# Kernel optimization log

Hardware: AMD Instinct MI355X
Metric: run time of the kernel (lower is better)

## Reference

```python
import jax, jax.numpy as jnp
import numpy as np

B, C, H, W = 8, 256, 128, 128
NUM_HEADS = 8
EPS = 1e-6


def setup_inputs() -> dict:
    key = jax.random.key(0)
    ks = jax.random.split(key, 7)
    s = 1.0 / np.sqrt(C)
    return {
        "x": jax.random.normal(ks[0], (B, C, H, W), dtype=jnp.float32),
        "Wq": jax.random.normal(ks[1], (C, C), dtype=jnp.float32) * s,
        "bq": jax.random.normal(ks[2], (C,), dtype=jnp.float32) * 0.01,
        "Wk": jax.random.normal(ks[3], (C, C), dtype=jnp.float32) * s,
        "bk": jax.random.normal(ks[4], (C,), dtype=jnp.float32) * 0.01,
        "Wv": jax.random.normal(ks[5], (C, C), dtype=jnp.float32) * s,
        "bv": jax.random.normal(ks[6], (C,), dtype=jnp.float32) * 0.01,
    }


def reference(x, Wq, bq, Wk, bk, Wv, bv):
    b, c_full, h_sp, w_sp = x.shape
    p = NUM_HEADS
    c = c_full // p  # per-head channels
    n = h_sp * w_sp  # spatial tokens

    def proj(Wm, bm):
        # 1x1 conv == channel-mixing linear: out[b,o,h,w] = sum_c W[o,c]*x[b,c,h,w] + b[o]
        return jnp.einsum('bchw,oc->bohw', x, Wm) + bm[None, :, None, None]

    q = jax.nn.softplus(proj(Wq, bq)).reshape(b, p, c, n).transpose(0, 1, 3, 2)  # [b,p,n,c]
    k = jax.nn.softplus(proj(Wk, bk)).reshape(b, p, c, n)                        # [b,p,c,n]
    v = proj(Wv, bv).reshape(b, p, c, n)                                         # [b,p,c,n]

    # KV accumulation: [b,p,c_k,c_v] (small)
    kv = jnp.einsum('bpmn,bpcn->bpmc', k, v)
    # normalization: 1 / (q . (sum_n k + eps))
    norm = 1.0 / jnp.einsum('bpnc,bpc->bpn', q, jnp.sum(k, axis=-1) + EPS)
    out = jnp.einsum('bpnm,bpmc,bpn->bpcn', q, kv, norm)  # [b,p,c,n]
    return out.reshape(b, c_full, h_sp, w_sp)
```

## Files before the change

kernel.cpp:

```cpp
#include <hip/hip_runtime.h>
#include <hip/hip_bf16.h>
#include <math.h>

#define BATCH 8
#define CFULL 256
#define HEADS 8
#define CH 32
#define NTOK 16384
#define TN 64
#define EPS 1e-6f

#define SWZ(tok) ((((tok) & 7) << 3) ^ ((((tok) >> 3) & 3) << 6))

typedef __bf16 bf16x8 __attribute__((ext_vector_type(8)));
typedef float f32x4 __attribute__((ext_vector_type(4)));
typedef float f32x16 __attribute__((ext_vector_type(16)));
typedef float fvec4 __attribute__((ext_vector_type(4)));
typedef unsigned short ushort8v __attribute__((ext_vector_type(8)));
typedef int int4v __attribute__((ext_vector_type(4)));

__device__ __forceinline__ unsigned short bf16bits(float f) {
    return __builtin_bit_cast(unsigned short, (__bf16)f);
}
__device__ __forceinline__ float softplus_f(float x) {
    return fmaxf(x, 0.0f) + __logf(1.0f + __expf(-fabsf(x)));
}

__device__ __forceinline__ void quad_transpose(fvec4& a, int lane) {
    const bool o1 = lane & 1, o2 = lane & 2;
    float s1 = o1 ? a.x : a.y; float g1 = __shfl_xor(s1, 1);
    float s2 = o1 ? a.z : a.w; float g2 = __shfl_xor(s2, 1);
    a.x = o1 ? g1 : a.x;  a.y = o1 ? a.y : g1;
    a.z = o1 ? g2 : a.z;  a.w = o1 ? a.w : g2;
    float s3 = o2 ? a.x : a.z; float g3 = __shfl_xor(s3, 2);
    float s4 = o2 ? a.y : a.w; float g4 = __shfl_xor(s4, 2);
    a.x = o2 ? g3 : a.x;  a.z = o2 ? a.z : g3;
    a.y = o2 ? g4 : a.y;  a.w = o2 ? a.w : g4;
}

template <int NW>
__device__ __forceinline__ void stage_x(const float* __restrict__ xb, int n0,
                                        unsigned short* xs, int wv, int lane) {
    const int q4 = lane & 3;
    const int t0 = (lane >> 2) << 2;
    constexpr int G = 64 / NW;
    #pragma unroll
    for (int g = 0; g < G; ++g) {
        const int c0 = wv * (G * 4) + g * 4;
        fvec4 a = __builtin_nontemporal_load(
            (const fvec4*)(xb + (size_t)(c0 + q4) * NTOK + n0 + t0));
        quad_transpose(a, lane);
        ushort4 pk;
        pk.x = bf16bits(a.x); pk.y = bf16bits(a.y);
        pk.z = bf16bits(a.z); pk.w = bf16bits(a.w);
        *(ushort4*)&xs[lane * CFULL + (c0 ^ SWZ(lane))] = pk;
    }
}

template <int NW>
__device__ __forceinline__ void stage_tile(const unsigned short* __restrict__ xTb,
                                           int n0, unsigned short* xs, int wv, int lane) {
    constexpr int R = 64 / NW;
    const unsigned short* src = xTb + (size_t)(n0 + wv * R) * CFULL + lane * 8;
    unsigned short* dst = &xs[wv * R * CFULL];
    #pragma unroll
    for (int i = 0; i < R / 2; ++i) {
        __builtin_amdgcn_global_load_lds(
            (const __attribute__((address_space(1))) unsigned int*)(src + i * 512),
            (__attribute__((address_space(3))) unsigned int*)(dst + i * 512),
            16, 0, 0);
    }
}

__global__ void prep_w(const float* __restrict__ Wq, const float* __restrict__ Wk,
                       const float* __restrict__ Wv, unsigned short* __restrict__ dst)
{
    const int i = blockIdx.x * 256 + threadIdx.x;
    const float* src = (i < 65536) ? Wq : ((i < 131072) ? Wk : Wv);
    dst[i] = bf16bits(src[i & 65535]);
}

__global__ __launch_bounds__(512)
void xpose(const float* __restrict__ x, unsigned short* __restrict__ xT)
{
    __shared__ __align__(16) unsigned short xs[TN * CFULL];
    const int tid = threadIdx.x;
    const int lane = tid & 63;
    const int wv = tid >> 6;
    const int b = blockIdx.x >> 8;
    const int n0 = (blockIdx.x & 255) * TN;

    stage_x<8>(x + (size_t)b * CFULL * NTOK, n0, xs, wv, lane);
    __syncthreads();
    int4v* dst = (int4v*)(xT + ((size_t)b * NTOK + n0) * CFULL);
    const int4v* src = (const int4v*)xs;
    #pragma unroll
    for (int i = 0; i < 4; ++i)
        dst[i * 512 + tid] = src[i * 512 + tid];
}

__global__ __launch_bounds__(512)
void k1_kv(const unsigned short* __restrict__ xT,
           const unsigned short* __restrict__ Wk,
           const unsigned short* __restrict__ Wv,
           const float* __restrict__ bk, const float* __restrict__ bv,
           float* __restrict__ kvpart, float* __restrict__ kspart,
           int bpb, int ntiles)
{
    __shared__ __align__(16) unsigned short xs[TN * CFULL];
    __shared__ __align__(16) unsigned short ks[CFULL * TN];

    const int tid = threadIdx.x;
    const int lane = tid & 63;
    const int wv = tid >> 6;
    const int l15 = lane & 15;
    const int lhi = lane >> 4;
    const int bid = blockIdx.x;
    const int b = bid / bpb;
    const int blk = bid % bpb;
    const unsigned short* xTb = xT + (size_t)b * NTOK * CFULL;

    float bkr[2], bvr[2];
    #pragma unroll
    for (int of = 0; of < 2; ++of) {
        bkr[of] = bk[wv * 32 + of * 16 + l15];
        bvr[of] = bv[wv * 32 + of * 16 + l15];
    }

    f32x16 kvacc = {};
    float ksum[2] = {0.f, 0.f};

    for (int t = 0; t < ntiles; ++t) {
        const int n0 = (blk * ntiles + t) * TN;
        __syncthreads();
        stage_tile<8>(xTb, n0, xs, wv, lane);
        __syncthreads();

        #pragma unroll
        for (int tfh = 0; tfh < 2; ++tfh) {
            f32x4 acc[2][2] = {};
            #pragma unroll
            for (int kk = 0; kk < 8; ++kk) {
                const int ch0 = kk * 32 + lhi * 8;
                bf16x8 af[2], bfr[2];
                #pragma unroll
                for (int tf = 0; tf < 2; ++tf) {
                    const int tok = (tfh * 2 + tf) * 16 + l15;
                    af[tf] = *(const bf16x8*)&xs[tok * CFULL + (ch0 ^ SWZ(tok))];
                }
                #pragma unroll
                for (int of = 0; of < 2; ++of) {
                    const int och = wv * 32 + of * 16 + l15;
                    bfr[of] = *(const bf16x8*)&Wk[och * CFULL + ch0];
                }
                #pragma unroll
                for (int tf = 0; tf < 2; ++tf)
                    #pragma unroll
                    for (int of = 0; of < 2; ++of)
                        acc[tf][of] = __builtin_amdgcn_mfma_f32_16x16x32_bf16(af[tf], bfr[of], acc[tf][of], 0, 0, 0);
            }
            #pragma unroll
            for (int tf = 0; tf < 2; ++tf) {
                #pragma unroll
                for (int of = 0; of < 2; ++of) {
                    const int och = wv * 32 + of * 16 + l15;
                    const float bias = bkr[of];
                    float v0 = softplus_f(acc[tf][of][0] + bias);
                    float v1 = softplus_f(acc[tf][of][1] + bias);
                    float v2 = softplus_f(acc[tf][of][2] + bias);
                    float v3 = softplus_f(acc[tf][of][3] + bias);
                    ksum[of] += v0 + v1 + v2 + v3;
                    ushort4 pk;
                    pk.x = bf16bits(v0); pk.y = bf16bits(v1);
                    pk.z = bf16bits(v2); pk.w = bf16bits(v3);
                    const int tok0 = (tfh * 2 + tf) * 16 + lhi * 4;
                    *(ushort4*)&ks[och * TN + (tok0 ^ ((och & 7) << 3))] = pk;
                }
            }
        }

        ushort4 vpk[4][2];
        #pragma unroll
        for (int tfh = 0; tfh < 2; ++tfh) {
            f32x4 acc[2][2] = {};
            #pragma unroll
            for (int kk = 0; kk < 8; ++kk) {
                const int ch0 = kk * 32 + lhi * 8;
                bf16x8 af[2], bfr[2];
                #pragma unroll
                for (int tf = 0; tf < 2; ++tf) {
                    const int tok = (tfh * 2 + tf) * 16 + l15;
                    af[tf] = *(const bf16x8*)&xs[tok * CFULL + (ch0 ^ SWZ(tok))];
                }
                #pragma unroll
                for (int of = 0; of < 2; ++of) {
                    const int och = wv * 32 + of * 16 + l15;
                    bfr[of] = *(const bf16x8*)&Wv[och * CFULL + ch0];
                }
                #pragma unroll
                for (int tf = 0; tf < 2; ++tf)
                    #pragma unroll
                    for (int of = 0; of < 2; ++of)
                        acc[tf][of] = __builtin_amdgcn_mfma_f32_16x16x32_bf16(af[tf], bfr[of], acc[tf][of], 0, 0, 0);
            }
            #pragma unroll
            for (int tf = 0; tf < 2; ++tf)
                #pragma unroll
                for (int of = 0; of < 2; ++of) {
                    const float bias = bvr[of];
                    vpk[tfh * 2 + tf][of].x = bf16bits(acc[tf][of][0] + bias);
                    vpk[tfh * 2 + tf][of].y = bf16bits(acc[tf][of][1] + bias);
                    vpk[tfh * 2 + tf][of].z = bf16bits(acc[tf][of][2] + bias);
                    vpk[tfh * 2 + tf][of].w = bf16bits(acc[tf][of][3] + bias);
                }
        }
        __syncthreads();
        #pragma unroll
        for (int tf = 0; tf < 4; ++tf)
            #pragma unroll
            for (int of = 0; of < 2; ++of) {
                const int och = wv * 32 + of * 16 + l15;
                const int tok0 = tf * 16 + lhi * 4;
                *(ushort4*)&xs[och * TN + (tok0 ^ ((och & 7) << 3))] = vpk[tf][of];
            }

        {
            const int l31 = lane & 31;
            const int tb = (lane >> 5) * 8;
            const int row = wv * 32 + l31;
            #pragma unroll
            for (int ts = 0; ts < 4; ++ts) {
                const int sw = (ts * 16 + tb) ^ ((row & 7) << 3);
                bf16x8 ak = *(const bf16x8*)&ks[row * TN + sw];
                bf16x8 av = *(const bf16x8*)&xs[row * TN + sw];
                kvacc = __builtin_amdgcn_mfma_f32_32x32x16_bf16(ak, av, kvacc, 0, 0, 0);
            }
        }
    }

    #pragma unroll
    for (int of = 0; of < 2; ++of) {
        float v = ksum[of];
        v += __shfl_xor(v, 16);
        v += __shfl_xor(v, 32);
        if (lhi == 0) kspart[bid * CFULL + wv * 32 + of * 16 + l15] = v;
    }
    {
        float* kvp = kvpart + ((size_t)bid << 13);
        const int l31 = lane & 31;
        const int hi = lane >> 5;
        #pragma unroll
        for (int q = 0; q < 4; ++q) {
            const int m0 = 8 * q + 4 * hi;
            f32x4 s;
            s[0] = kvacc[4 * q + 0]; s[1] = kvacc[4 * q + 1];
            s[2] = kvacc[4 * q + 2]; s[3] = kvacc[4 * q + 3];
            *(f32x4*)&kvp[wv * 1024 + l31 * 32 + m0] = s;
        }
    }
}

__global__ __launch_bounds__(256)
void k1r(const float* __restrict__ kvpart, const float* __restrict__ kspart,
         unsigned short* __restrict__ kvT, float* __restrict__ kse, int bpb)
{
    const int o = blockIdx.x * 256 + threadIdx.x;
    const int b = o >> 13;
    const int r = o & 8191;
    float s = 0.f;
    for (int j = 0; j < bpb; ++j)
        s += kvpart[((size_t)(b * bpb + j) << 13) + r];
    kvT[o] = bf16bits(s);
    if (blockIdx.x < BATCH) {
        const int bb = blockIdx.x;
        float t = 0.f;
        for (int j = 0; j < bpb; ++j)
            t += kspart[(bb * bpb + j) * CFULL + threadIdx.x];
        kse[bb * CFULL + threadIdx.x] = t + EPS;
    }
}

__global__ __launch_bounds__(512)
void k2_out(const unsigned short* __restrict__ xT,
            const unsigned short* __restrict__ Wq,
            const float* __restrict__ bq,
            const unsigned short* __restrict__ kvT, const float* __restrict__ ksef,
            float* __restrict__ outp)
{
    __shared__ __align__(16) unsigned short xs[TN * CFULL];
    __shared__ float kse[CFULL];
    __shared__ float normls[HEADS][TN];

    const int tid = threadIdx.x;
    const int lane = tid & 63;
    const int wv = tid >> 6;
    const int l15 = lane & 15;
    const int lhi = lane >> 4;
    const int b = blockIdx.x >> 8;
    const int blk = blockIdx.x & 255;
    const int n0 = blk * TN;
    float* ob = outp + (size_t)b * CFULL * NTOK;

    stage_tile<8>(xT + (size_t)b * NTOK * CFULL, n0, xs, wv, lane);

    if (tid < CFULL) kse[tid] = ksef[b * CFULL + tid];

    float bq0[2][4];
    #pragma unroll
    for (int of = 0; of < 2; ++of) {
        const int och0 = wv * 32 + of * 16 + lhi * 4;
        #pragma unroll
        for (int r = 0; r < 4; ++r) bq0[of][r] = bq[och0 + r];
    }

    __syncthreads();

    ushort4 qpk[2][4];
    {
        f32x4 acc[2][4] = {};
        #pragma unroll
        for (int kk = 0; kk < 8; ++kk) {
            const int ch0 = kk * 32 + lhi * 8;
            bf16x8 aw[2], bx[4];
            #pragma unroll
            for (int of = 0; of < 2; ++of)
                aw[of] = *(const bf16x8*)&Wq[(wv * 32 + of * 16 + l15) * CFULL + ch0];
            #pragma unroll
            for (int nf = 0; nf < 4; ++nf) {
                const int tok = nf * 16 + l15;
                bx[nf] = *(const bf16x8*)&xs[tok * CFULL + (ch0 ^ SWZ(tok))];
            }
            #pragma unroll
            for (int of = 0; of < 2; ++of)
                #pragma unroll
                for (int nf = 0; nf < 4; ++nf)
                    acc[of][nf] = __builtin_amdgcn_mfma_f32_16x16x32_bf16(aw[of], bx[nf], acc[of][nf], 0, 0, 0);
        }
        #pragma unroll
        for (int of = 0; of < 2; ++of) {
            #pragma unroll
            for (int nf = 0; nf < 4; ++nf) {
                qpk[of][nf].x = bf16bits(softplus_f(acc[of][nf][0] + bq0[of][0]));
                qpk[of][nf].y = bf16bits(softplus_f(acc[of][nf][1] + bq0[of][1]));
                qpk[of][nf].z = bf16bits(softplus_f(acc[of][nf][2] + bq0[of][2]));
                qpk[of][nf].w = bf16bits(softplus_f(acc[of][nf][3] + bq0[of][3]));
            }
        }
    }
    __syncthreads();
    #pragma unroll
    for (int of = 0; of < 2; ++of)
        #pragma unroll
        for (int nf = 0; nf < 4; ++nf) {
            const int tok = nf * 16 + l15;
            const int och0 = wv * 32 + of * 16 + lhi * 4;
            *(ushort4*)&xs[tok * CFULL + (och0 ^ SWZ(tok))] = qpk[of][nf];
        }

    {
        float d = 0.f;
        #pragma unroll
        for (int mg = 0; mg < 4; ++mg) {
            bf16x8 qv = *(const bf16x8*)&xs[lane * CFULL + ((wv * 32 + mg * 8) ^ SWZ(lane))];
            #pragma unroll
            for (int j = 0; j < 8; ++j)
                d += (float)qv[j] * kse[wv * 32 + mg * 8 + j];
        }
        normls[wv][lane] = 1.0f / d;
    }

    bf16x8 bh[2];
    {
        const int base = (b * HEADS + wv) << 10;
        #pragma unroll
        for (int hf = 0; hf < 2; ++hf)
            bh[hf] = *(const bf16x8*)&kvT[base + (hf * 16 + l15) * 32 + lhi * 8];
    }

    #pragma unroll
    for (int nf = 0; nf < 4; ++nf) {
        const int tok = nf * 16 + l15;
        bf16x8 af = *(const bf16x8*)&xs[tok * CFULL + ((wv * 32 + lhi * 8) ^ SWZ(tok))];
        f32x4 oA = {}, oB = {};
        oA = __builtin_amdgcn_mfma_f32_16x16x32_bf16(af, bh[0], oA, 0, 0, 0);
        oB = __builtin_amdgcn_mfma_f32_16x16x32_bf16(af, bh[1], oB, 0, 0, 0);
        const int tb = nf * 16 + lhi * 4;
        f32x4 sA, sB;
        sA[0] = oA[0] * normls[wv][tb + 0]; sA[1] = oA[1] * normls[wv][tb + 1];
        sA[2] = oA[2] * normls[wv][tb + 2]; sA[3] = oA[3] * normls[wv][tb + 3];
        sB[0] = oB[0] * normls[wv][tb + 0]; sB[1] = oB[1] * normls[wv][tb + 1];
        sB[2] = oB[2] * normls[wv][tb + 2]; sB[3] = oB[3] * normls[wv][tb + 3];
        __builtin_nontemporal_store(sA, (f32x4*)&ob[(size_t)(wv * 32 + l15) * NTOK + n0 + tb]);
        __builtin_nontemporal_store(sB, (f32x4*)&ob[(size_t)(wv * 32 + 16 + l15) * NTOK + n0 + tb]);
    }
}

extern "C" void kernel_launch(void* const* d_in, const int* in_sizes, int n_in,
                              void* d_out, int out_size, void* d_ws, size_t ws_size,
                              hipStream_t stream)
{
    const float* x  = (const float*)d_in[0];
    const float* Wq = (const float*)d_in[1];
    const float* bq = (const float*)d_in[2];
    const float* Wk = (const float*)d_in[3];
    const float* bk = (const float*)d_in[4];
    const float* Wv = (const float*)d_in[5];
    const float* bv = (const float*)d_in[6];
    float* out = (float*)d_out;

    unsigned char* ws = (unsigned char*)d_ws;
    unsigned short* wbf = (unsigned short*)ws;
    unsigned short* kvT = (unsigned short*)(ws + 393216);
    float* kse = (float*)(ws + 524288);

    const size_t xT_sz = (size_t)BATCH * NTOK * CFULL * 2;

    int bpb = 64;
    size_t ksp_off = 532480;
    size_t kvp_off = ksp_off + (size_t)BATCH * bpb * CFULL * 4;
    size_t kvp_sz  = (size_t)BATCH * bpb * 8192 * 4;
    if (ws_size < kvp_off + kvp_sz + xT_sz) {
        bpb = 16;
        kvp_off = ksp_off + (size_t)BATCH * bpb * CFULL * 4;
        kvp_sz  = (size_t)BATCH * bpb * 8192 * 4;
    }
    float* kspart = (float*)(ws + ksp_off);
    float* kvpart = (float*)(ws + kvp_off);
    unsigned short* xT = (unsigned short*)(ws + kvp_off + kvp_sz);
    const int ntiles = NTOK / TN / bpb;

    hipLaunchKernelGGL(prep_w, dim3(768), dim3(256), 0, stream, Wq, Wk, Wv, wbf);
    hipLaunchKernelGGL(xpose, dim3(BATCH * 256), dim3(512), 0, stream, x, xT);
    hipLaunchKernelGGL(k1_kv, dim3(BATCH * bpb), dim3(512), 0, stream,
                       xT, wbf + 65536, wbf + 2 * 65536, bk, bv,
                       kvpart, kspart, bpb, ntiles);
    hipLaunchKernelGGL(k1r, dim3(256), dim3(256), 0, stream,
                       kvpart, kspart, kvT, kse, bpb);
    hipLaunchKernelGGL(k2_out, dim3(BATCH * 256), dim3(512), 0, stream,
                       xT, wbf, bq, kvT, kse, out);
}
```

Baseline: 219.2 us.

## Double-buffer 32-token x tiles in k1_kv with async LDS prefetch

The KV accumulation kernel now works on 32-token tiles held in two LDS buffers. The next tile is fetched with global_load_lds while the current one is computed, so each iteration needs only one barrier instead of the earlier stage-then-sync sequence. K and V projections are written to separate padded LDS buffers (row stride 40) instead of XOR swizzling, and V no longer overwrites the x buffer. This is meant to hide global load latency and remove barriers. In exchange it uses more LDS and runs twice as many loop iterations, each doing smaller MFMA work.

New measurement: 213.0 us. 1.03x faster.

```diff
diff --git a/kernel.cpp b/kernel.cpp
--- a/kernel.cpp
+++ b/kernel.cpp
@@ -8,6 +8,8 @@
 #define CH 32
 #define NTOK 16384
 #define TN 64
+#define TTN 32
+#define KSLD 40
 #define EPS 1e-6f
 
 #define SWZ(tok) ((((tok) & 7) << 3) ^ ((((tok) >> 3) & 3) << 6))
@@ -72,6 +74,19 @@
     }
 }
 
+__device__ __forceinline__ void stage32(const unsigned short* __restrict__ xTb,
+                                        int n0, unsigned short* buf, int wv, int lane) {
+    const unsigned short* src = xTb + (size_t)(n0 + wv * 4) * CFULL + lane * 8;
+    unsigned short* dst = buf + wv * 4 * CFULL;
+    #pragma unroll
+    for (int i = 0; i < 2; ++i) {
+        __builtin_amdgcn_global_load_lds(
+            (const __attribute__((address_space(1))) unsigned int*)(src + i * 512),
+            (__attribute__((address_space(3))) unsigned int*)(dst + i * 512),
+            16, 0, 0);
+    }
+}
+
 __global__ void prep_w(const float* __restrict__ Wq, const float* __restrict__ Wk,
                        const float* __restrict__ Wv, unsigned short* __restrict__ dst)
 {
@@ -107,8 +122,10 @@
            float* __restrict__ kvpart, float* __restrict__ kspart,
            int bpb, int ntiles)
 {
-    __shared__ __align__(16) unsigned short xs[TN * CFULL];
-    __shared__ __align__(16) unsigned short ks[CFULL * TN];
+    __shared__ __align__(16) unsigned short xs0[TTN * CFULL];
+    __shared__ __align__(16) unsigned short xs1[TTN * CFULL];
+    __shared__ __align__(16) unsigned short ks[CFULL * KSLD];
+    __shared__ __align__(16) unsigned short vs[CFULL * KSLD];
 
     const int tid = threadIdx.x;
     const int lane = tid & 63;
@@ -118,6 +135,7 @@
     const int bid = blockIdx.x;
     const int b = bid / bpb;
     const int blk = bid % bpb;
+    const int tokbase = blk * (ntiles * TTN);
     const unsigned short* xTb = xT + (size_t)b * NTOK * CFULL;
 
     float bkr[2], bvr[2];
@@ -130,14 +148,16 @@
     f32x16 kvacc = {};
     float ksum[2] = {0.f, 0.f};
 
+    stage32(xTb, tokbase, xs0, wv, lane);
+    __syncthreads();
+
     for (int t = 0; t < ntiles; ++t) {
-        const int n0 = (blk * ntiles + t) * TN;
-        __syncthreads();
-        stage_tile<8>(xTb, n0, xs, wv, lane);
-        __syncthreads();
-
-        #pragma unroll
-        for (int tfh = 0; tfh < 2; ++tfh) {
+        unsigned short* cur = (t & 1) ? xs1 : xs0;
+        unsigned short* nxt = (t & 1) ? xs0 : xs1;
+        if (t + 1 < ntiles)
+            stage32(xTb, tokbase + (t + 1) * TTN, nxt, wv, lane);
+
+        {
             f32x4 acc[2][2] = {};
             #pragma unroll
             for (int kk = 0; kk < 8; ++kk) {
@@ -145,8 +165,8 @@
                 bf16x8 af[2], bfr[2];
                 #pragma unroll
                 for (int tf = 0; tf < 2; ++tf) {
-                    const int tok = (tfh * 2 + tf) * 16 + l15;
-                    af[tf] = *(const bf16x8*)&xs[tok * CFULL + (ch0 ^ SWZ(tok))];
+                    const int tok = tf * 16 + l15;
+                    af[tf] = *(const bf16x8*)&cur[tok * CFULL + (ch0 ^ SWZ(tok))];
                 }
                 #pragma unroll
                 for (int of = 0; of < 2; ++of) {
@@ -173,15 +193,12 @@
                     ushort4 pk;
                     pk.x = bf16bits(v0); pk.y = bf16bits(v1);
                     pk.z = bf16bits(v2); pk.w = bf16bits(v3);
-                    const int tok0 = (tfh * 2 + tf) * 16 + lhi * 4;
-                    *(ushort4*)&ks[och * TN + (tok0 ^ ((och & 7) << 3))] = pk;
-                }
-            }
-        }
-
-        ushort4 vpk[4][2];
-        #pragma unroll
-        for (int tfh = 0; tfh < 2; ++tfh) {
+                    *(ushort4*)&ks[och * KSLD + tf * 16 + lhi * 4] = pk;
+                }
+            }
+        }
+
+        {
             f32x4 acc[2][2] = {};
             #pragma unroll
             for (int kk = 0; kk < 8; ++kk) {
@@ -189,8 +206,8 @@
                 bf16x8 af[2], bfr[2];
                 #pragma unroll
                 for (int tf = 0; tf < 2; ++tf) {
-                    const int tok = (tfh * 2 + tf) * 16 + l15;
-                    af[tf] = *(const bf16x8*)&xs[tok * CFULL + (ch0 ^ SWZ(tok))];
+                    const int tok = tf * 16 + l15;
+                    af[tf] = *(const bf16x8*)&cur[tok * CFULL + (ch0 ^ SWZ(tok))];
                 }
                 #pragma unroll
                 for (int of = 0; of < 2; ++of) {
@@ -204,38 +221,35 @@
                         acc[tf][of] = __builtin_amdgcn_mfma_f32_16x16x32_bf16(af[tf], bfr[of], acc[tf][of], 0, 0, 0);
             }
             #pragma unroll
-            for (int tf = 0; tf < 2; ++tf)
+            for (int tf = 0; tf < 2; ++tf) {
                 #pragma unroll
                 for (int of = 0; of < 2; ++of) {
+                    const int och = wv * 32 + of * 16 + l15;
                     const float bias = bvr[of];
-                    vpk[tfh * 2 + tf][of].x = bf16bits(acc[tf][of][0] + bias);
-                    vpk[tfh * 2 + tf][of].y = bf16bits(acc[tf][of][1] + bias);
-                    vpk[tfh * 2 + tf][of].z = bf16bits(acc[tf][of][2] + bias);
-                    vpk[tfh * 2 + tf][of].w = bf16bits(acc[tf][of][3] + bias);
-                }
-        }
-        __syncthreads();
-        #pragma unroll
-        for (int tf = 0; tf < 4; ++tf)
-            #pragma unroll
-            for (int of = 0; of < 2; ++of) {
-                const int och = wv * 32 + of * 16 + l15;
-                const int tok0 = tf * 16 + lhi * 4;
-                *(ushort4*)&xs[och * TN + (tok0 ^ ((och & 7) << 3))] = vpk[tf][of];
-            }
+                    ushort4 pk;
+                    pk.x = bf16bits(acc[tf][of][0] + bias);
+                    pk.y = bf16bits(acc[tf][of][1] + bias);
+                    pk.z = bf16bits(acc[tf][of][2] + bias);
+                    pk.w = bf16bits(acc[tf][of][3] + bias);
+                    *(ushort4*)&vs[och * KSLD + tf * 16 + lhi * 4] = pk;
+                }
+            }
+        }
 
         {
             const int l31 = lane & 31;
-            const int tb = (lane >> 5) * 8;
+            const int hi = lane >> 5;
             const int row = wv * 32 + l31;
             #pragma unroll
-            for (int ts = 0; ts < 4; ++ts) {
-                const int sw = (ts * 16 + tb) ^ ((row & 7) << 3);
-                bf16x8 ak = *(const bf16x8*)&ks[row * TN + sw];
-                bf16x8 av = *(const bf16x8*)&xs[row * TN + sw];
+            for (int ts = 0; ts < 2; ++ts) {
+                const int sw = ts * 16 + hi * 8;
+                bf16x8 ak = *(const bf16x8*)&ks[row * KSLD + sw];
+                bf16x8 av = *(const bf16x8*)&vs[row * KSLD + sw];
                 kvacc = __builtin_amdgcn_mfma_f32_32x32x16_bf16(ak, av, kvacc, 0, 0, 0);
             }
         }
+
+        __syncthreads();
     }
 
     #pragma unroll
@@ -427,7 +441,7 @@
     float* kspart = (float*)(ws + ksp_off);
     float* kvpart = (float*)(ws + kvp_off);
     unsigned short* xT = (unsigned short*)(ws + kvp_off + kvp_sz);
-    const int ntiles = NTOK / TN / bpb;
+    const int ntiles = NTOK / TTN / bpb;
 
     hipLaunchKernelGGL(prep_w, dim3(768), dim3(256), 0, stream, Wq, Wk, Wv, wbf);
     hipLaunchKernelGGL(xpose, dim3(BATCH * 256), dim3(512), 0, stream, x, xT);
```
